# Optimization experiments

Measured on AMD Instinct MI355X. Metric: run time of the kernel, lower is better.

Reference implementation:

```python
import jax, jax.numpy as jnp
import numpy as np

DIM = 3            # point feature dim (xyz)
POS_HID = 64       # pos_mlp hidden
ATTN_HID = DIM * 4 # attn_mlp hidden (mult=4)
N_NBR = 16         # points per group
GROUPS = 512       # groups per batch element
MLP_D = N_NBR * DIM  # 48


def setup_inputs() -> dict:
    key = jax.random.key(0)
    ks = jax.random.split(key, 20)
    B = 32
    s = lambda *sh: 1.0 / np.sqrt(sh[0])
    inp = {
        "original_points": jax.random.normal(ks[0], (B, GROUPS, DIM), jnp.float32),
        "data": jax.random.normal(ks[1], (B, GROUPS, N_NBR, DIM), jnp.float32),
        # PointTransformerLayer params
        "w_qkv": jax.random.normal(ks[2], (DIM, DIM * 3), jnp.float32) * s(DIM),
        "pos_w1": jax.random.normal(ks[3], (3, POS_HID), jnp.float32) * s(3),
        "pos_b1": jnp.zeros((POS_HID,), jnp.float32),
        "pos_w2": jax.random.normal(ks[4], (POS_HID, DIM), jnp.float32) * s(POS_HID),
        "pos_b2": jnp.zeros((DIM,), jnp.float32),
        "attn_w1": jax.random.normal(ks[5], (DIM, ATTN_HID), jnp.float32) * s(DIM),
        "attn_b1": jnp.zeros((ATTN_HID,), jnp.float32),
        "attn_w2": jax.random.normal(ks[6], (ATTN_HID, DIM), jnp.float32) * s(ATTN_HID),
        "attn_b2": jnp.zeros((DIM,), jnp.float32),
        # downstream MLP params
        "mlp_w1": jax.random.normal(ks[7], (MLP_D, MLP_D), jnp.float32) * s(MLP_D),
        "mlp_b1": jnp.zeros((MLP_D,), jnp.float32),
        "mlp_w2": jax.random.normal(ks[8], (MLP_D, MLP_D), jnp.float32) * s(MLP_D),
        "mlp_b2": jnp.zeros((MLP_D,), jnp.float32),
        "mlp_w3": jax.random.normal(ks[9], (MLP_D, 1), jnp.float32) * s(MLP_D),
        "mlp_b3": jnp.zeros((1,), jnp.float32),
    }
    return inp


def reference(original_points, data, w_qkv, pos_w1, pos_b1, pos_w2, pos_b2,
              attn_w1, attn_b1, attn_w2, attn_b2,
              mlp_w1, mlp_b1, mlp_w2, mlp_b2, mlp_w3, mlp_b3):
    B, G, n, d = data.shape
    x = data.reshape(B * G, n, d)          # (BG, n, 3)
    pos = x[:, :, :3]                       # pos == features here (f=3)

    # Point-transformer vector attention
    qkv = x @ w_qkv                          # (BG, n, 9)
    q, k, v = jnp.split(qkv, 3, axis=-1)
    rel_pos = pos[:, :, None, :] - pos[:, None, :, :]              # (BG, n, n, 3)
    rel_emb = jax.nn.relu(rel_pos @ pos_w1 + pos_b1) @ pos_w2 + pos_b2  # (BG, n, n, 3)
    qk_rel = q[:, :, None, :] - k[:, None, :, :]                   # (BG, n, n, 3)
    v_ij = v[:, None, :, :] + rel_emb                              # (BG, n, n, 3)
    sim = jax.nn.relu((qk_rel + rel_emb) @ attn_w1 + attn_b1) @ attn_w2 + attn_b2
    attn = jax.nn.softmax(sim, axis=-2)                            # softmax over j
    agg = jnp.einsum('bijd,bijd->bid', attn, v_ij)                 # (BG, n, 3)

    # regroup into (B, 512, 48) exactly as stack(split(512, dim=0))
    sa = agg.reshape(B, G, n * d)
    h = jax.nn.relu(sa @ mlp_w1 + mlp_b1)
    h = jax.nn.relu(h @ mlp_w2 + mlp_b2)
    return h @ mlp_w3 + mlp_b3              # (B, 512, 1)
```

## Files before the change

### kernel.cpp

```cpp
#include <hip/hip_runtime.h>


typedef _Float16 h2 __attribute__((ext_vector_type(2)));
typedef _Float16 h8 __attribute__((ext_vector_type(8)));

#define AH_STRIDE 36

union H8U { h8 v; h2 p[4]; unsigned u[4]; };

__device__ __forceinline__ h2 pkrtz(float a, float b) {
    return __builtin_bit_cast(h2, __builtin_amdgcn_cvt_pkrtz(a, b));
}
__device__ __forceinline__ h2 uash2(unsigned u) {
    return __builtin_bit_cast(h2, u);
}
__device__ __forceinline__ h2 hmax2(h2 a, h2 b) {
    return __builtin_elementwise_max(a, b);
}

#if __has_builtin(__builtin_amdgcn_fdot2)
__device__ __forceinline__ float dot2acc(h2 a, h2 b, float c) {
    return __builtin_amdgcn_fdot2(a, b, c, false);
}
#else
__device__ __forceinline__ float dot2acc(h2 a, h2 b, float c) {
    return fmaf((float)a.x, (float)b.x, fmaf((float)a.y, (float)b.y, c));
}
#endif

__device__ __forceinline__ float dpp_add16(float x) {
    float s = x;
    int t;
    t = __builtin_amdgcn_update_dpp(0, __builtin_bit_cast(int, s), 0x121, 0xf, 0xf, false);
    s += __builtin_bit_cast(float, t);
    t = __builtin_amdgcn_update_dpp(0, __builtin_bit_cast(int, s), 0x122, 0xf, 0xf, false);
    s += __builtin_bit_cast(float, t);
    t = __builtin_amdgcn_update_dpp(0, __builtin_bit_cast(int, s), 0x124, 0xf, 0xf, false);
    s += __builtin_bit_cast(float, t);
    t = __builtin_amdgcn_update_dpp(0, __builtin_bit_cast(int, s), 0x128, 0xf, 0xf, false);
    s += __builtin_bit_cast(float, t);
    return s;
}

__global__ void wpack(const float* __restrict__ pw2, const float* __restrict__ aw1,
                      const float* __restrict__ ab1, const float* __restrict__ aw2,
                      unsigned* __restrict__ ws) {
    const int t = threadIdx.x;
    if (t < 96) {
        const int hp = t & 31, c = t >> 5;
        ws[c*32+hp] = __builtin_bit_cast(unsigned, pkrtz(pw2[(2*hp)*3+c], pw2[(2*hp+1)*3+c]));
    } else if (t < 114) {
        const int idx = t - 96, r = idx / 6, gp = idx % 6;
        ws[96+r*6+gp] = __builtin_bit_cast(unsigned, pkrtz(aw1[r*12+2*gp], aw1[r*12+2*gp+1]));
    } else if (t < 120) {
        const int gp = t - 114;
        ws[114+gp] = __builtin_bit_cast(unsigned, pkrtz(ab1[2*gp], ab1[2*gp+1]));
    } else if (t < 138) {
        const int idx = t - 120, gp = idx / 3, c = idx % 3;
        ws[120+gp*3+c] = __builtin_bit_cast(unsigned, pkrtz(aw2[(2*gp)*3+c], aw2[(2*gp+1)*3+c]));
    }
}

__global__ __launch_bounds__(256) void pt_main(
    const float* __restrict__ data,
    const float* __restrict__ wqkv,
    const float* __restrict__ pw1,
    const float* __restrict__ pb1,
    const float* __restrict__ pb2,
    const float* __restrict__ ab2,
    const float* __restrict__ mw1,
    const float* __restrict__ mb1,
    const float* __restrict__ mw2,
    const float* __restrict__ mb2,
    const float* __restrict__ mw3,
    const float* __restrict__ mb3,
    const unsigned* __restrict__ wsp,
    float* __restrict__ out)
{
    __shared__ __attribute__((aligned(16))) float s_q4[2][64], s_k4[2][64], s_v4[2][64];
    __shared__ __attribute__((aligned(16))) float s_sa[2][48];
    __shared__ __attribute__((aligned(16))) float s_h1[2][48];
    __shared__ __attribute__((aligned(16))) unsigned s_a1h[2][16 * AH_STRIDE];
    __shared__ __attribute__((aligned(16))) unsigned s_a2h[2][16 * AH_STRIDE];

    const int t   = threadIdx.x;
    const int grp = t >> 7;
    const int lt  = t & 127;
    const int g   = blockIdx.x * 2 + grp;

    if (lt < 48) {
        const int sec = lt >> 4, p = lt & 15;
        const float x0 = data[g*48 + p*3 + 0];
        const float x1 = data[g*48 + p*3 + 1];
        const float x2 = data[g*48 + p*3 + 2];
        float* dst = (sec == 0) ? s_q4[grp] : (sec == 1) ? s_k4[grp] : s_v4[grp];
        #pragma unroll
        for (int c = 0; c < 3; ++c) {
            dst[p*4+c] = fmaf(x0, wqkv[0*9 + sec*3 + c],
                         fmaf(x1, wqkv[1*9 + sec*3 + c],
                         x2 * wqkv[2*9 + sec*3 + c]));
        }
        dst[p*4+3] = 0.0f;
    }

    {
        const int p  = lt >> 3;
        const int hc = (lt & 7) << 3;
        const float x0 = data[g*48 + p*3 + 0];
        const float x1 = data[g*48 + p*3 + 1];
        const float x2 = data[g*48 + p*3 + 2];
        const float4 w0a = *(const float4*)&pw1[hc],     w0b = *(const float4*)&pw1[hc+4];
        const float4 w1a = *(const float4*)&pw1[64+hc],  w1b = *(const float4*)&pw1[64+hc+4];
        const float4 w2a = *(const float4*)&pw1[128+hc], w2b = *(const float4*)&pw1[128+hc+4];
        const float4 ba  = *(const float4*)&pb1[hc],     bb  = *(const float4*)&pb1[hc+4];
        float s[8];
        #pragma unroll
        for (int c = 0; c < 4; ++c) {
            s[c]   = fmaf(x0, (&w0a.x)[c], fmaf(x1, (&w1a.x)[c], x2 * (&w2a.x)[c]));
            s[4+c] = fmaf(x0, (&w0b.x)[c], fmaf(x1, (&w1b.x)[c], x2 * (&w2b.x)[c]));
        }
        uint4 a1u, a2u;
        a1u.x = __builtin_bit_cast(unsigned, pkrtz(s[0]+ba.x, s[1]+ba.y));
        a1u.y = __builtin_bit_cast(unsigned, pkrtz(s[2]+ba.z, s[3]+ba.w));
        a1u.z = __builtin_bit_cast(unsigned, pkrtz(s[4]+bb.x, s[5]+bb.y));
        a1u.w = __builtin_bit_cast(unsigned, pkrtz(s[6]+bb.z, s[7]+bb.w));
        a2u.x = __builtin_bit_cast(unsigned, pkrtz(s[0], s[1]));
        a2u.y = __builtin_bit_cast(unsigned, pkrtz(s[2], s[3]));
        a2u.z = __builtin_bit_cast(unsigned, pkrtz(s[4], s[5]));
        a2u.w = __builtin_bit_cast(unsigned, pkrtz(s[6], s[7]));
        const int base = p * AH_STRIDE + (hc >> 1);
        *(uint4*)&s_a1h[grp][base] = a1u;
        *(uint4*)&s_a2h[grp][base] = a2u;
    }
    __syncthreads();

    const int i = lt >> 4, j = lt & 15, i2 = i + 8;

    float eA0 = pb2[0], eA1 = pb2[1], eA2 = pb2[2];
    float eB0 = pb2[0], eB1 = pb2[1], eB2 = pb2[2];
    #pragma unroll
    for (int cc = 0; cc < 8; ++cc) {
        H8U aiA, aiB, aj;
        aiA.v = *(const h8*)&s_a1h[grp][i  * AH_STRIDE + cc*4];
        aiB.v = *(const h8*)&s_a1h[grp][i2 * AH_STRIDE + cc*4];
        aj.v  = *(const h8*)&s_a2h[grp][j  * AH_STRIDE + cc*4];
        #pragma unroll
        for (int m = 0; m < 4; ++m) {
            const int hp = cc*4 + m;
            const h2 z = {(_Float16)0, (_Float16)0};
            const h2 w0 = uash2(wsp[0*32+hp]);
            const h2 w1 = uash2(wsp[1*32+hp]);
            const h2 w2 = uash2(wsp[2*32+hp]);
            h2 rA = hmax2(aiA.p[m] - aj.p[m], z);
            h2 rB = hmax2(aiB.p[m] - aj.p[m], z);
            eA0 = dot2acc(rA, w0, eA0);
            eA1 = dot2acc(rA, w1, eA1);
            eA2 = dot2acc(rA, w2, eA2);
            eB0 = dot2acc(rB, w0, eB0);
            eB1 = dot2acc(rB, w1, eB1);
            eB2 = dot2acc(rB, w2, eB2);
        }
    }

    const float4 qA = *(const float4*)&s_q4[grp][i*4];
    const float4 qB = *(const float4*)&s_q4[grp][i2*4];
    const float4 kv = *(const float4*)&s_k4[grp][j*4];
    const float4 vv = *(const float4*)&s_v4[grp][j*4];

    const float viA0 = vv.x + eA0, viA1 = vv.y + eA1, viA2 = vv.z + eA2;
    const float viB0 = vv.x + eB0, viB1 = vv.y + eB1, viB2 = vv.z + eB2;
    const float siA0 = qA.x - kv.x + eA0, siA1 = qA.y - kv.y + eA1, siA2 = qA.z - kv.z + eA2;
    const float siB0 = qB.x - kv.x + eB0, siB1 = qB.y - kv.y + eB1, siB2 = qB.z - kv.z + eB2;

    const h2 z2 = {(_Float16)0, (_Float16)0};
    const h2 sAx = pkrtz(siA0, siA0), sAy = pkrtz(siA1, siA1), sAz = pkrtz(siA2, siA2);
    const h2 sBx = pkrtz(siB0, siB0), sBy = pkrtz(siB1, siB1), sBz = pkrtz(siB2, siB2);
    float mA0 = ab2[0], mA1 = ab2[1], mA2 = ab2[2];
    float mB0 = ab2[0], mB1 = ab2[1], mB2 = ab2[2];
    #pragma unroll
    for (int gp = 0; gp < 6; ++gp) {
        const h2 b1p = uash2(wsp[114+gp]);
        const h2 u0 = uash2(wsp[96+0*6+gp]);
        const h2 u1 = uash2(wsp[96+1*6+gp]);
        const h2 u2 = uash2(wsp[96+2*6+gp]);
        const h2 v0 = uash2(wsp[120+gp*3+0]);
        const h2 v1 = uash2(wsp[120+gp*3+1]);
        const h2 v2 = uash2(wsp[120+gp*3+2]);
        h2 accA = b1p, accB = b1p;
        accA = __builtin_elementwise_fma(sAx, u0, accA);
        accA = __builtin_elementwise_fma(sAy, u1, accA);
        accA = __builtin_elementwise_fma(sAz, u2, accA);
        accB = __builtin_elementwise_fma(sBx, u0, accB);
        accB = __builtin_elementwise_fma(sBy, u1, accB);
        accB = __builtin_elementwise_fma(sBz, u2, accB);
        h2 hA = hmax2(accA, z2), hB = hmax2(accB, z2);
        mA0 = dot2acc(hA, v0, mA0);
        mA1 = dot2acc(hA, v1, mA1);
        mA2 = dot2acc(hA, v2, mA2);
        mB0 = dot2acc(hB, v0, mB0);
        mB1 = dot2acc(hB, v1, mB1);
        mB2 = dot2acc(hB, v2, mB2);
    }

    const float L2E = 1.44269504f;
    const float pA0 = __builtin_amdgcn_exp2f(mA0 * L2E);
    const float pA1 = __builtin_amdgcn_exp2f(mA1 * L2E);
    const float pA2 = __builtin_amdgcn_exp2f(mA2 * L2E);
    const float pB0 = __builtin_amdgcn_exp2f(mB0 * L2E);
    const float pB1 = __builtin_amdgcn_exp2f(mB1 * L2E);
    const float pB2 = __builtin_amdgcn_exp2f(mB2 * L2E);

    const float nA0 = dpp_add16(pA0 * viA0);
    const float nA1 = dpp_add16(pA1 * viA1);
    const float nA2 = dpp_add16(pA2 * viA2);
    const float dA0 = dpp_add16(pA0);
    const float dA1 = dpp_add16(pA1);
    const float dA2 = dpp_add16(pA2);
    const float nB0 = dpp_add16(pB0 * viB0);
    const float nB1 = dpp_add16(pB1 * viB1);
    const float nB2 = dpp_add16(pB2 * viB2);
    const float dB0 = dpp_add16(pB0);
    const float dB1 = dpp_add16(pB1);
    const float dB2 = dpp_add16(pB2);

    if (j == 0) {
        s_sa[grp][i*3+0]  = nA0 * __builtin_amdgcn_rcpf(dA0);
        s_sa[grp][i*3+1]  = nA1 * __builtin_amdgcn_rcpf(dA1);
        s_sa[grp][i*3+2]  = nA2 * __builtin_amdgcn_rcpf(dA2);
        s_sa[grp][i2*3+0] = nB0 * __builtin_amdgcn_rcpf(dB0);
        s_sa[grp][i2*3+1] = nB1 * __builtin_amdgcn_rcpf(dB1);
        s_sa[grp][i2*3+2] = nB2 * __builtin_amdgcn_rcpf(dB2);
    }
    __syncthreads();

    if (lt < 48) {
        const int o = lt;
        float a0 = 0.f, a1 = 0.f, a2 = 0.f, a3 = 0.f;
        #pragma unroll
        for (int c = 0; c < 48; c += 4) {
            const float4 sa = *(const float4*)&s_sa[grp][c];
            a0 = fmaf(sa.x, mw1[(c+0)*48+o], a0);
            a1 = fmaf(sa.y, mw1[(c+1)*48+o], a1);
            a2 = fmaf(sa.z, mw1[(c+2)*48+o], a2);
            a3 = fmaf(sa.w, mw1[(c+3)*48+o], a3);
        }
        s_h1[grp][o] = fmaxf((a0+a1) + (a2+a3) + mb1[o], 0.0f);
        __builtin_amdgcn_wave_barrier();
        float b0 = 0.f, b1 = 0.f, b2 = 0.f, b3 = 0.f;
        #pragma unroll
        for (int c = 0; c < 48; c += 4) {
            const float4 hh = *(const float4*)&s_h1[grp][c];
            b0 = fmaf(hh.x, mw2[(c+0)*48+o], b0);
            b1 = fmaf(hh.y, mw2[(c+1)*48+o], b1);
            b2 = fmaf(hh.z, mw2[(c+2)*48+o], b2);
            b3 = fmaf(hh.w, mw2[(c+3)*48+o], b3);
        }
        const float h2v = fmaxf((b0+b1) + (b2+b3) + mb2[o], 0.0f);
        const float fv = h2v * mw3[o];
        const float r = dpp_add16(fv);
        const int ri = __builtin_bit_cast(int, r);
        const float tot =
            __builtin_bit_cast(float, __builtin_amdgcn_readlane(ri, 0)) +
            __builtin_bit_cast(float, __builtin_amdgcn_readlane(ri, 16)) +
            __builtin_bit_cast(float, __builtin_amdgcn_readlane(ri, 32));
        if (o == 0) out[g] = tot + mb3[0];
    }
}

extern "C" void kernel_launch(void* const* d_in, const int* in_sizes, int n_in,
                              void* d_out, int out_size, void* d_ws, size_t ws_size,
                              hipStream_t stream) {
    const float* data = (const float*)d_in[1];
    unsigned* ws = (unsigned*)d_ws;
    const int groups = out_size;

    wpack<<<1, 256, 0, stream>>>(
        (const float*)d_in[5],
        (const float*)d_in[7],
        (const float*)d_in[8],
        (const float*)d_in[9],
        ws);

    pt_main<<<groups / 2, 256, 0, stream>>>(
        data,
        (const float*)d_in[2],
        (const float*)d_in[3],
        (const float*)d_in[4],
        (const float*)d_in[6],
        (const float*)d_in[10],
        (const float*)d_in[11],
        (const float*)d_in[12],
        (const float*)d_in[13],
        (const float*)d_in[14],
        (const float*)d_in[15],
        (const float*)d_in[16],
        ws,
        (float*)d_out);
}
```

Baseline: 136.9 us.

## Map one group per wavefront and replace block barriers with wave barriers

Each 64-lane wavefront now processes a whole point group, so a 256-thread block handles four groups instead of two. The block-wide __syncthreads calls become wave barriers, and each lane loops over two halves of the attention rows, computing four query rows per lane instead of two. This removes block-level synchronisation and puts the MLP tail on a fully used wave. In exchange, each lane does twice the serial attention work and the launch has half as many blocks.

After: 138.4 us. About the same (+1.1%).

```diff
diff --git a/kernel.cpp b/kernel.cpp
--- a/kernel.cpp
+++ b/kernel.cpp
@@ -77,23 +77,23 @@
     const unsigned* __restrict__ wsp,
     float* __restrict__ out)
 {
-    __shared__ __attribute__((aligned(16))) float s_q4[2][64], s_k4[2][64], s_v4[2][64];
-    __shared__ __attribute__((aligned(16))) float s_sa[2][48];
-    __shared__ __attribute__((aligned(16))) float s_h1[2][48];
-    __shared__ __attribute__((aligned(16))) unsigned s_a1h[2][16 * AH_STRIDE];
-    __shared__ __attribute__((aligned(16))) unsigned s_a2h[2][16 * AH_STRIDE];
-
-    const int t   = threadIdx.x;
-    const int grp = t >> 7;
-    const int lt  = t & 127;
-    const int g   = blockIdx.x * 2 + grp;
-
-    if (lt < 48) {
-        const int sec = lt >> 4, p = lt & 15;
+    __shared__ __attribute__((aligned(16))) float s_q4[4][64], s_k4[4][64], s_v4[4][64];
+    __shared__ __attribute__((aligned(16))) float s_sa[4][48];
+    __shared__ __attribute__((aligned(16))) float s_h1[4][48];
+    __shared__ __attribute__((aligned(16))) unsigned s_a1h[4][16 * AH_STRIDE];
+    __shared__ __attribute__((aligned(16))) unsigned s_a2h[4][16 * AH_STRIDE];
+
+    const int t  = threadIdx.x;
+    const int wv = t >> 6;
+    const int ln = t & 63;
+    const int g  = blockIdx.x * 4 + wv;
+
+    if (ln < 48) {
+        const int sec = ln >> 4, p = ln & 15;
         const float x0 = data[g*48 + p*3 + 0];
         const float x1 = data[g*48 + p*3 + 1];
         const float x2 = data[g*48 + p*3 + 2];
-        float* dst = (sec == 0) ? s_q4[grp] : (sec == 1) ? s_k4[grp] : s_v4[grp];
+        float* dst = (sec == 0) ? s_q4[wv] : (sec == 1) ? s_k4[wv] : s_v4[wv];
         #pragma unroll
         for (int c = 0; c < 3; ++c) {
             dst[p*4+c] = fmaf(x0, wqkv[0*9 + sec*3 + c],
@@ -104,152 +104,155 @@
     }
 
     {
-        const int p  = lt >> 3;
-        const int hc = (lt & 7) << 3;
+        const int p  = ln & 15;
+        const int qd = ln >> 4;
+        const int hc = qd << 4;
         const float x0 = data[g*48 + p*3 + 0];
         const float x1 = data[g*48 + p*3 + 1];
         const float x2 = data[g*48 + p*3 + 2];
-        const float4 w0a = *(const float4*)&pw1[hc],     w0b = *(const float4*)&pw1[hc+4];
-        const float4 w1a = *(const float4*)&pw1[64+hc],  w1b = *(const float4*)&pw1[64+hc+4];
-        const float4 w2a = *(const float4*)&pw1[128+hc], w2b = *(const float4*)&pw1[128+hc+4];
-        const float4 ba  = *(const float4*)&pb1[hc],     bb  = *(const float4*)&pb1[hc+4];
-        float s[8];
-        #pragma unroll
-        for (int c = 0; c < 4; ++c) {
-            s[c]   = fmaf(x0, (&w0a.x)[c], fmaf(x1, (&w1a.x)[c], x2 * (&w2a.x)[c]));
-            s[4+c] = fmaf(x0, (&w0b.x)[c], fmaf(x1, (&w1b.x)[c], x2 * (&w2b.x)[c]));
-        }
-        uint4 a1u, a2u;
-        a1u.x = __builtin_bit_cast(unsigned, pkrtz(s[0]+ba.x, s[1]+ba.y));
-        a1u.y = __builtin_bit_cast(unsigned, pkrtz(s[2]+ba.z, s[3]+ba.w));
-        a1u.z = __builtin_bit_cast(unsigned, pkrtz(s[4]+bb.x, s[5]+bb.y));
-        a1u.w = __builtin_bit_cast(unsigned, pkrtz(s[6]+bb.z, s[7]+bb.w));
-        a2u.x = __builtin_bit_cast(unsigned, pkrtz(s[0], s[1]));
-        a2u.y = __builtin_bit_cast(unsigned, pkrtz(s[2], s[3]));
-        a2u.z = __builtin_bit_cast(unsigned, pkrtz(s[4], s[5]));
-        a2u.w = __builtin_bit_cast(unsigned, pkrtz(s[6], s[7]));
-        const int base = p * AH_STRIDE + (hc >> 1);
-        *(uint4*)&s_a1h[grp][base] = a1u;
-        *(uint4*)&s_a2h[grp][base] = a2u;
-    }
-    __syncthreads();
-
-    const int i = lt >> 4, j = lt & 15, i2 = i + 8;
-
-    float eA0 = pb2[0], eA1 = pb2[1], eA2 = pb2[2];
-    float eB0 = pb2[0], eB1 = pb2[1], eB2 = pb2[2];
+        float s[16];
+        #pragma unroll
+        for (int c = 0; c < 16; ++c) {
+            const int h = hc + c;
+            s[c] = fmaf(x0, pw1[h], fmaf(x1, pw1[64+h], x2 * pw1[128+h]));
+        }
+        uint4 a1u0, a1u1, a2u0, a2u1;
+        #pragma unroll
+        for (int d = 0; d < 4; ++d) {
+            const int c = d * 2;
+            (&a1u0.x)[d] = __builtin_bit_cast(unsigned, pkrtz(s[c]   + pb1[hc+c],   s[c+1] + pb1[hc+c+1]));
+            (&a1u1.x)[d] = __builtin_bit_cast(unsigned, pkrtz(s[8+c] + pb1[hc+8+c], s[9+c] + pb1[hc+9+c]));
+            (&a2u0.x)[d] = __builtin_bit_cast(unsigned, pkrtz(s[c],   s[c+1]));
+            (&a2u1.x)[d] = __builtin_bit_cast(unsigned, pkrtz(s[8+c], s[9+c]));
+        }
+        const int base = p * AH_STRIDE + (qd << 3);
+        *(uint4*)&s_a1h[wv][base]     = a1u0;
+        *(uint4*)&s_a1h[wv][base + 4] = a1u1;
+        *(uint4*)&s_a2h[wv][base]     = a2u0;
+        *(uint4*)&s_a2h[wv][base + 4] = a2u1;
+    }
+    __builtin_amdgcn_wave_barrier();
+
+    const int j = ln & 15, q = ln >> 4;
+    const float4 kv = *(const float4*)&s_k4[wv][j*4];
+    const float4 vv = *(const float4*)&s_v4[wv][j*4];
+    const float L2E = 1.44269504f;
+    const h2 z2 = {(_Float16)0, (_Float16)0};
+
     #pragma unroll
-    for (int cc = 0; cc < 8; ++cc) {
-        H8U aiA, aiB, aj;
-        aiA.v = *(const h8*)&s_a1h[grp][i  * AH_STRIDE + cc*4];
-        aiB.v = *(const h8*)&s_a1h[grp][i2 * AH_STRIDE + cc*4];
-        aj.v  = *(const h8*)&s_a2h[grp][j  * AH_STRIDE + cc*4];
-        #pragma unroll
-        for (int m = 0; m < 4; ++m) {
-            const int hp = cc*4 + m;
-            const h2 z = {(_Float16)0, (_Float16)0};
-            const h2 w0 = uash2(wsp[0*32+hp]);
-            const h2 w1 = uash2(wsp[1*32+hp]);
-            const h2 w2 = uash2(wsp[2*32+hp]);
-            h2 rA = hmax2(aiA.p[m] - aj.p[m], z);
-            h2 rB = hmax2(aiB.p[m] - aj.p[m], z);
-            eA0 = dot2acc(rA, w0, eA0);
-            eA1 = dot2acc(rA, w1, eA1);
-            eA2 = dot2acc(rA, w2, eA2);
-            eB0 = dot2acc(rB, w0, eB0);
-            eB1 = dot2acc(rB, w1, eB1);
-            eB2 = dot2acc(rB, w2, eB2);
-        }
-    }
-
-    const float4 qA = *(const float4*)&s_q4[grp][i*4];
-    const float4 qB = *(const float4*)&s_q4[grp][i2*4];
-    const float4 kv = *(const float4*)&s_k4[grp][j*4];
-    const float4 vv = *(const float4*)&s_v4[grp][j*4];
-
-    const float viA0 = vv.x + eA0, viA1 = vv.y + eA1, viA2 = vv.z + eA2;
-    const float viB0 = vv.x + eB0, viB1 = vv.y + eB1, viB2 = vv.z + eB2;
-    const float siA0 = qA.x - kv.x + eA0, siA1 = qA.y - kv.y + eA1, siA2 = qA.z - kv.z + eA2;
-    const float siB0 = qB.x - kv.x + eB0, siB1 = qB.y - kv.y + eB1, siB2 = qB.z - kv.z + eB2;
-
-    const h2 z2 = {(_Float16)0, (_Float16)0};
-    const h2 sAx = pkrtz(siA0, siA0), sAy = pkrtz(siA1, siA1), sAz = pkrtz(siA2, siA2);
-    const h2 sBx = pkrtz(siB0, siB0), sBy = pkrtz(siB1, siB1), sBz = pkrtz(siB2, siB2);
-    float mA0 = ab2[0], mA1 = ab2[1], mA2 = ab2[2];
-    float mB0 = ab2[0], mB1 = ab2[1], mB2 = ab2[2];
-    #pragma unroll
-    for (int gp = 0; gp < 6; ++gp) {
-        const h2 b1p = uash2(wsp[114+gp]);
-        const h2 u0 = uash2(wsp[96+0*6+gp]);
-        const h2 u1 = uash2(wsp[96+1*6+gp]);
-        const h2 u2 = uash2(wsp[96+2*6+gp]);
-        const h2 v0 = uash2(wsp[120+gp*3+0]);
-        const h2 v1 = uash2(wsp[120+gp*3+1]);
-        const h2 v2 = uash2(wsp[120+gp*3+2]);
-        h2 accA = b1p, accB = b1p;
-        accA = __builtin_elementwise_fma(sAx, u0, accA);
-        accA = __builtin_elementwise_fma(sAy, u1, accA);
-        accA = __builtin_elementwise_fma(sAz, u2, accA);
-        accB = __builtin_elementwise_fma(sBx, u0, accB);
-        accB = __builtin_elementwise_fma(sBy, u1, accB);
-        accB = __builtin_elementwise_fma(sBz, u2, accB);
-        h2 hA = hmax2(accA, z2), hB = hmax2(accB, z2);
-        mA0 = dot2acc(hA, v0, mA0);
-        mA1 = dot2acc(hA, v1, mA1);
-        mA2 = dot2acc(hA, v2, mA2);
-        mB0 = dot2acc(hB, v0, mB0);
-        mB1 = dot2acc(hB, v1, mB1);
-        mB2 = dot2acc(hB, v2, mB2);
-    }
-
-    const float L2E = 1.44269504f;
-    const float pA0 = __builtin_amdgcn_exp2f(mA0 * L2E);
-    const float pA1 = __builtin_amdgcn_exp2f(mA1 * L2E);
-    const float pA2 = __builtin_amdgcn_exp2f(mA2 * L2E);
-    const float pB0 = __builtin_amdgcn_exp2f(mB0 * L2E);
-    const float pB1 = __builtin_amdgcn_exp2f(mB1 * L2E);
-    const float pB2 = __builtin_amdgcn_exp2f(mB2 * L2E);
-
-    const float nA0 = dpp_add16(pA0 * viA0);
-    const float nA1 = dpp_add16(pA1 * viA1);
-    const float nA2 = dpp_add16(pA2 * viA2);
-    const float dA0 = dpp_add16(pA0);
-    const float dA1 = dpp_add16(pA1);
-    const float dA2 = dpp_add16(pA2);
-    const float nB0 = dpp_add16(pB0 * viB0);
-    const float nB1 = dpp_add16(pB1 * viB1);
-    const float nB2 = dpp_add16(pB2 * viB2);
-    const float dB0 = dpp_add16(pB0);
-    const float dB1 = dpp_add16(pB1);
-    const float dB2 = dpp_add16(pB2);
-
-    if (j == 0) {
-        s_sa[grp][i*3+0]  = nA0 * __builtin_amdgcn_rcpf(dA0);
-        s_sa[grp][i*3+1]  = nA1 * __builtin_amdgcn_rcpf(dA1);
-        s_sa[grp][i*3+2]  = nA2 * __builtin_amdgcn_rcpf(dA2);
-        s_sa[grp][i2*3+0] = nB0 * __builtin_amdgcn_rcpf(dB0);
-        s_sa[grp][i2*3+1] = nB1 * __builtin_amdgcn_rcpf(dB1);
-        s_sa[grp][i2*3+2] = nB2 * __builtin_amdgcn_rcpf(dB2);
-    }
-    __syncthreads();
-
-    if (lt < 48) {
-        const int o = lt;
+    for (int half = 0; half < 2; ++half) {
+        const int iA = q + 8*half, iB = iA + 4;
+
+        float eA0 = pb2[0], eA1 = pb2[1], eA2 = pb2[2];
+        float eB0 = pb2[0], eB1 = pb2[1], eB2 = pb2[2];
+        #pragma unroll
+        for (int cc = 0; cc < 8; ++cc) {
+            H8U aiA, aiB, aj;
+            aiA.v = *(const h8*)&s_a1h[wv][iA * AH_STRIDE + cc*4];
+            aiB.v = *(const h8*)&s_a1h[wv][iB * AH_STRIDE + cc*4];
+            aj.v  = *(const h8*)&s_a2h[wv][j  * AH_STRIDE + cc*4];
+            #pragma unroll
+            for (int m = 0; m < 4; ++m) {
+                const int hp = cc*4 + m;
+                const h2 w0 = uash2(wsp[0*32+hp]);
+                const h2 w1 = uash2(wsp[1*32+hp]);
+                const h2 w2 = uash2(wsp[2*32+hp]);
+                h2 rA = hmax2(aiA.p[m] - aj.p[m], z2);
+                h2 rB = hmax2(aiB.p[m] - aj.p[m], z2);
+                eA0 = dot2acc(rA, w0, eA0);
+                eA1 = dot2acc(rA, w1, eA1);
+                eA2 = dot2acc(rA, w2, eA2);
+                eB0 = dot2acc(rB, w0, eB0);
+                eB1 = dot2acc(rB, w1, eB1);
+                eB2 = dot2acc(rB, w2, eB2);
+            }
+        }
+
+        const float4 qA = *(const float4*)&s_q4[wv][iA*4];
+        const float4 qB = *(const float4*)&s_q4[wv][iB*4];
+
+        const float viA0 = vv.x + eA0, viA1 = vv.y + eA1, viA2 = vv.z + eA2;
+        const float viB0 = vv.x + eB0, viB1 = vv.y + eB1, viB2 = vv.z + eB2;
+        const float siA0 = qA.x - kv.x + eA0, siA1 = qA.y - kv.y + eA1, siA2 = qA.z - kv.z + eA2;
+        const float siB0 = qB.x - kv.x + eB0, siB1 = qB.y - kv.y + eB1, siB2 = qB.z - kv.z + eB2;
+
+        const h2 sAx = pkrtz(siA0, siA0), sAy = pkrtz(siA1, siA1), sAz = pkrtz(siA2, siA2);
+        const h2 sBx = pkrtz(siB0, siB0), sBy = pkrtz(siB1, siB1), sBz = pkrtz(siB2, siB2);
+        float mA0 = ab2[0], mA1 = ab2[1], mA2 = ab2[2];
+        float mB0 = ab2[0], mB1 = ab2[1], mB2 = ab2[2];
+        #pragma unroll
+        for (int gp = 0; gp < 6; ++gp) {
+            const h2 b1p = uash2(wsp[114+gp]);
+            const h2 u0 = uash2(wsp[96+0*6+gp]);
+            const h2 u1 = uash2(wsp[96+1*6+gp]);
+            const h2 u2 = uash2(wsp[96+2*6+gp]);
+            const h2 v0 = uash2(wsp[120+gp*3+0]);
+            const h2 v1 = uash2(wsp[120+gp*3+1]);
+            const h2 v2 = uash2(wsp[120+gp*3+2]);
+            h2 accA = b1p, accB = b1p;
+            accA = __builtin_elementwise_fma(sAx, u0, accA);
+            accA = __builtin_elementwise_fma(sAy, u1, accA);
+            accA = __builtin_elementwise_fma(sAz, u2, accA);
+            accB = __builtin_elementwise_fma(sBx, u0, accB);
+            accB = __builtin_elementwise_fma(sBy, u1, accB);
+            accB = __builtin_elementwise_fma(sBz, u2, accB);
+            h2 hA = hmax2(accA, z2), hB = hmax2(accB, z2);
+            mA0 = dot2acc(hA, v0, mA0);
+            mA1 = dot2acc(hA, v1, mA1);
+            mA2 = dot2acc(hA, v2, mA2);
+            mB0 = dot2acc(hB, v0, mB0);
+            mB1 = dot2acc(hB, v1, mB1);
+            mB2 = dot2acc(hB, v2, mB2);
+        }
+
+        const float pA0 = __builtin_amdgcn_exp2f(mA0 * L2E);
+        const float pA1 = __builtin_amdgcn_exp2f(mA1 * L2E);
+        const float pA2 = __builtin_amdgcn_exp2f(mA2 * L2E);
+        const float pB0 = __builtin_amdgcn_exp2f(mB0 * L2E);
+        const float pB1 = __builtin_amdgcn_exp2f(mB1 * L2E);
+        const float pB2 = __builtin_amdgcn_exp2f(mB2 * L2E);
+
+        const float nA0 = dpp_add16(pA0 * viA0);
+        const float nA1 = dpp_add16(pA1 * viA1);
+        const float nA2 = dpp_add16(pA2 * viA2);
+        const float dA0 = dpp_add16(pA0);
+        const float dA1 = dpp_add16(pA1);
+        const float dA2 = dpp_add16(pA2);
+        const float nB0 = dpp_add16(pB0 * viB0);
+        const float nB1 = dpp_add16(pB1 * viB1);
+        const float nB2 = dpp_add16(pB2 * viB2);
+        const float dB0 = dpp_add16(pB0);
+        const float dB1 = dpp_add16(pB1);
+        const float dB2 = dpp_add16(pB2);
+
+        if (j == 0) {
+            s_sa[wv][iA*3+0] = nA0 * __builtin_amdgcn_rcpf(dA0);
+            s_sa[wv][iA*3+1] = nA1 * __builtin_amdgcn_rcpf(dA1);
+            s_sa[wv][iA*3+2] = nA2 * __builtin_amdgcn_rcpf(dA2);
+            s_sa[wv][iB*3+0] = nB0 * __builtin_amdgcn_rcpf(dB0);
+            s_sa[wv][iB*3+1] = nB1 * __builtin_amdgcn_rcpf(dB1);
+            s_sa[wv][iB*3+2] = nB2 * __builtin_amdgcn_rcpf(dB2);
+        }
+    }
+    __builtin_amdgcn_wave_barrier();
+
+    if (ln < 48) {
+        const int o = ln;
         float a0 = 0.f, a1 = 0.f, a2 = 0.f, a3 = 0.f;
         #pragma unroll
         for (int c = 0; c < 48; c += 4) {
-            const float4 sa = *(const float4*)&s_sa[grp][c];
+            const float4 sa = *(const float4*)&s_sa[wv][c];
             a0 = fmaf(sa.x, mw1[(c+0)*48+o], a0);
             a1 = fmaf(sa.y, mw1[(c+1)*48+o], a1);
             a2 = fmaf(sa.z, mw1[(c+2)*48+o], a2);
             a3 = fmaf(sa.w, mw1[(c+3)*48+o], a3);
         }
-        s_h1[grp][o] = fmaxf((a0+a1) + (a2+a3) + mb1[o], 0.0f);
+        s_h1[wv][o] = fmaxf((a0+a1) + (a2+a3) + mb1[o], 0.0f);
         __builtin_amdgcn_wave_barrier();
         float b0 = 0.f, b1 = 0.f, b2 = 0.f, b3 = 0.f;
         #pragma unroll
         for (int c = 0; c < 48; c += 4) {
-            const float4 hh = *(const float4*)&s_h1[grp][c];
+            const float4 hh = *(const float4*)&s_h1[wv][c];
             b0 = fmaf(hh.x, mw2[(c+0)*48+o], b0);
             b1 = fmaf(hh.y, mw2[(c+1)*48+o], b1);
             b2 = fmaf(hh.z, mw2[(c+2)*48+o], b2);
@@ -281,7 +284,7 @@
         (const float*)d_in[9],
         ws);
 
-    pt_main<<<groups / 2, 256, 0, stream>>>(
+    pt_main<<<groups / 4, 256, 0, stream>>>(
         data,
         (const float*)d_in[2],
         (const float*)d_in[3],
```
